# Kernel tuning notes

Measured on AMD Instinct MI355X. Metric: run time of the kernel, lower is better.

## Reference

```python
import jax, jax.numpy as jnp
import numpy as np

H = 2048  # hidden_size
I = 8192  # intermediate_size
B, S = 4, 2048


def setup_inputs() -> dict:
    key = jax.random.key(0)
    ks = jax.random.split(key, 8)
    scale = 1.0 / np.sqrt(H)
    scale_i = 1.0 / np.sqrt(I)
    x = jax.random.normal(ks[0], (B, S, H), dtype=jnp.float32)
    mask = jax.random.randint(ks[1], (B, S), 0, 2) > 0  # bool per-token routing
    # torch nn.Linear weights are [out_features, in_features]
    w1 = jax.random.normal(ks[2], (I, H), dtype=jnp.float32) * scale
    w2 = jax.random.normal(ks[3], (H, I), dtype=jnp.float32) * scale_i
    w3 = jax.random.normal(ks[4], (I, H), dtype=jnp.float32) * scale
    u1 = jax.random.normal(ks[5], (I, H), dtype=jnp.float32) * scale
    u2 = jax.random.normal(ks[6], (H, I), dtype=jnp.float32) * scale_i
    u3 = jax.random.normal(ks[7], (I, H), dtype=jnp.float32) * scale
    return {"x": x, "mask": mask, "w1": w1, "w2": w2, "w3": w3,
            "u1": u1, "u2": u2, "u3": u3}


def reference(x, mask, w1, w2, w3, u1, u2, u3):
    # branch 1 SwiGLU: silu(x @ w1^T) * (x @ w3^T), then w2
    proj1 = jax.nn.silu(jnp.einsum('bsh,ih->bsi', x, w1)) * jnp.einsum('bsh,ih->bsi', x, w3)
    proj2 = jax.nn.silu(jnp.einsum('bsh,ih->bsi', x, u1)) * jnp.einsum('bsh,ih->bsi', x, u3)
    out1 = jnp.einsum('bsi,hi->bsh', proj1, w2)
    out2 = jnp.einsum('bsi,hi->bsh', proj2, u2)
    m = mask[:, :, None]
    return jnp.where(m, out1, out2)
```

## Files before the change

### kernel.cpp

```cpp
#include <hip/hip_runtime.h>
#include <hip/hip_bf16.h>
#include <stdint.h>

#define DIM_H 2048
#define DIM_I 8192
#define TOKENS 8192
#define RB256 34
#define CROWS (RB256*256)

typedef __attribute__((ext_vector_type(8))) short bf16x8;
typedef __attribute__((ext_vector_type(4))) float f32x4;

#define MF(a,b,c) __builtin_amdgcn_mfma_f32_16x16x32_bf16((a),(b),(c),0,0,0)

__device__ __forceinline__ unsigned short f2bf(float f) {
    union { float f; unsigned u; } v; v.f = f;
    return (unsigned short)((v.u + 0x7FFF + ((v.u >> 16) & 1)) >> 16);
}

__global__ __launch_bounds__(256) void cvt_kernel(const float* __restrict__ in,
                                                  unsigned short* __restrict__ out,
                                                  int n4) {
    int stride = gridDim.x * blockDim.x;
    for (int j = blockIdx.x * blockDim.x + threadIdx.x; j < n4; j += stride) {
        float4 v = reinterpret_cast<const float4*>(in)[j];
        ushort4 o;
        o.x = f2bf(v.x); o.y = f2bf(v.y); o.z = f2bf(v.z); o.w = f2bf(v.w);
        reinterpret_cast<ushort4*>(out)[j] = o;
    }
}

__global__ __launch_bounds__(256) void cvt13_kernel(const float* __restrict__ w1,
                                                    const float* __restrict__ w3,
                                                    unsigned short* __restrict__ W13,
                                                    int n4) {
    int stride = gridDim.x * blockDim.x;
    for (int j = blockIdx.x * blockDim.x + threadIdx.x; j < n4; j += stride) {
        int flat = j << 2;
        int R = flat >> 11;
        int col = flat & 2047;
        int orow = ((R >> 4) << 5) | (R & 15);
        float4 v1 = reinterpret_cast<const float4*>(w1)[j];
        float4 v3 = reinterpret_cast<const float4*>(w3)[j];
        ushort4 o1, o3;
        o1.x=f2bf(v1.x); o1.y=f2bf(v1.y); o1.z=f2bf(v1.z); o1.w=f2bf(v1.w);
        o3.x=f2bf(v3.x); o3.y=f2bf(v3.y); o3.z=f2bf(v3.z); o3.w=f2bf(v3.w);
        *reinterpret_cast<ushort4*>(&W13[(size_t)orow * DIM_H + col]) = o1;
        *reinterpret_cast<ushort4*>(&W13[(size_t)(orow + 16) * DIM_H + col]) = o3;
    }
}

__global__ __launch_bounds__(256) void compact_kernel(const int* __restrict__ mask,
                                                      int* __restrict__ idx,
                                                      int* __restrict__ hdr) {
    __shared__ int cnt[256];
    const int t = threadIdx.x;
    const int base = t * 32;
    unsigned bits = 0;
#pragma unroll
    for (int j = 0; j < 32; ++j)
        if (mask[base + j] != 0) bits |= (1u << j);
    const int c = __popc(bits);
    cnt[t] = c;
    __syncthreads();
    for (int off = 1; off < 256; off <<= 1) {
        int v = cnt[t];
        int add = (t >= off) ? cnt[t - off] : 0;
        __syncthreads();
        cnt[t] = v + add;
        __syncthreads();
    }
    const int Mw  = cnt[255];
    const int MwP = (Mw + 255) & ~255;
    const int Mu  = TOKENS - Mw;
    const int MuP = (Mu + 255) & ~255;

    for (int j = t; j < CROWS; j += 256) idx[j] = -1;
    __syncthreads();

    int pw = cnt[t] - c;
    int pz = base - pw;
#pragma unroll
    for (int j = 0; j < 32; ++j) {
        int tok = base + j;
        if ((bits >> j) & 1) idx[pw++] = tok;
        else                 idx[MwP + pz++] = tok;
    }
    if (t == 0) {
        hdr[0] = MwP >> 8;
        hdr[1] = (MwP + MuP) >> 8;
        hdr[2] = Mw;
        hdr[3] = Mu;
    }
}


#define LDF4(D0,D1,D2,D3, SB, RB) do { \
    const unsigned short* _sl = &smem[(SB)]; \
    D0 = *reinterpret_cast<const bf16x8*>(&_sl[((RB) +  0)*32 + c16r]); \
    D1 = *reinterpret_cast<const bf16x8*>(&_sl[((RB) + 16)*32 + c16r]); \
    D2 = *reinterpret_cast<const bf16x8*>(&_sl[((RB) + 32)*32 + c16r]); \
    D3 = *reinterpret_cast<const bf16x8*>(&_sl[((RB) + 48)*32 + c16r]); \
} while(0)

#define STAGE2(UB_, S0_, S1_, KOFS_) do { \
    __builtin_amdgcn_global_load_lds((const __attribute__((address_space(1))) void*)((S0_) + (KOFS_)), \
        (__attribute__((address_space(3))) void*)&smem[(UB_) + wave*512], 16, 0, 0); \
    __builtin_amdgcn_global_load_lds((const __attribute__((address_space(1))) void*)((S1_) + (KOFS_)), \
        (__attribute__((address_space(3))) void*)&smem[(UB_) + 4096 + wave*512], 16, 0, 0); \
} while(0)

#define MFMA32() do { \
  __builtin_amdgcn_s_setprio(1); \
  acc[0][0]=MF(af0,bfr0,acc[0][0]); acc[0][1]=MF(af0,bfr1,acc[0][1]); acc[0][2]=MF(af0,bfr2,acc[0][2]); acc[0][3]=MF(af0,bfr3,acc[0][3]); \
  acc[1][0]=MF(af1,bfr0,acc[1][0]); acc[1][1]=MF(af1,bfr1,acc[1][1]); acc[1][2]=MF(af1,bfr2,acc[1][2]); acc[1][3]=MF(af1,bfr3,acc[1][3]); \
  acc[2][0]=MF(af2,bfr0,acc[2][0]); acc[2][1]=MF(af2,bfr1,acc[2][1]); acc[2][2]=MF(af2,bfr2,acc[2][2]); acc[2][3]=MF(af2,bfr3,acc[2][3]); \
  acc[3][0]=MF(af3,bfr0,acc[3][0]); acc[3][1]=MF(af3,bfr1,acc[3][1]); acc[3][2]=MF(af3,bfr2,acc[3][2]); acc[3][3]=MF(af3,bfr3,acc[3][3]); \
  acc[4][0]=MF(af4,bfr0,acc[4][0]); acc[4][1]=MF(af4,bfr1,acc[4][1]); acc[4][2]=MF(af4,bfr2,acc[4][2]); acc[4][3]=MF(af4,bfr3,acc[4][3]); \
  acc[5][0]=MF(af5,bfr0,acc[5][0]); acc[5][1]=MF(af5,bfr1,acc[5][1]); acc[5][2]=MF(af5,bfr2,acc[5][2]); acc[5][3]=MF(af5,bfr3,acc[5][3]); \
  acc[6][0]=MF(af6,bfr0,acc[6][0]); acc[6][1]=MF(af6,bfr1,acc[6][1]); acc[6][2]=MF(af6,bfr2,acc[6][2]); acc[6][3]=MF(af6,bfr3,acc[6][3]); \
  acc[7][0]=MF(af7,bfr0,acc[7][0]); acc[7][1]=MF(af7,bfr1,acc[7][1]); acc[7][2]=MF(af7,bfr2,acc[7][2]); acc[7][3]=MF(af7,bfr3,acc[7][3]); \
  __builtin_amdgcn_s_setprio(0); \
} while(0)

#define VMB() do { \
    asm volatile("s_waitcnt vmcnt(8)" ::: "memory"); \
    __builtin_amdgcn_s_barrier(); \
} while(0)

#define PHASE(ABASE, BBASE, SA_UB, SB_UB, KO) do { \
    LDF4(af0,af1,af2,af3, (ABASE), rAb); \
    LDF4(af4,af5,af6,af7, (ABASE), rAb + 64); \
    LDF4(bfr0,bfr1,bfr2,bfr3, (BBASE), rBb); \
    STAGE2((SA_UB), sa0, sa1, (KO)); \
    STAGE2((SB_UB), sb0, sb1, (KO)); \
    MFMA32(); \
    VMB(); \
} while(0)

#define KLOOP(NT) do { \
    STAGE2(0,     sa0, sa1, 0);   STAGE2(16384, sb0, sb1, 0);    \
    STAGE2(8192,  sa0, sa1, 32);  STAGE2(24576, sb0, sb1, 32);   \
    STAGE2(32768, sa0, sa1, 64);  STAGE2(49152, sb0, sb1, 64);   \
    VMB(); \
    for (int s = 0; s < (NT)/2; ++s) { \
         \
        PHASE(0,             16384,         32768 + 8192,  32768 + 24576, 96);    \
        PHASE(8192,          24576,         0,             16384,         128);   \
         \
        PHASE(32768,         32768 + 16384, 8192,          24576,         160);   \
        PHASE(32768 + 8192,  32768 + 24576, 32768,         32768 + 16384, 192);   \
        sa0 += 128; sa1 += 128; sb0 += 128; sb1 += 128; \
    } \
} while(0)

__global__ __launch_bounds__(512, 2) void gemm1_kernel(
    const unsigned short* __restrict__ xb,
    const unsigned short* __restrict__ W13,
    const unsigned short* __restrict__ U13,
    const int* __restrict__ idx, const int* __restrict__ hdr,
    unsigned short* __restrict__ P)
{
    __shared__ __align__(16) unsigned short smem[65536];
    const int wB  = hdr[0];
    const int rbT = hdr[1];
    const int nwg = gridDim.x;
    const int q8  = nwg >> 3;
    const int swzb = ((int)blockIdx.x & 7) * q8 + ((int)blockIdx.x >> 3);
    const int rb = swzb % RB256;
    const int bx = swzb / RB256;
    if (rb >= rbT) return;
    const unsigned short* Bm = (rb < wB) ? W13 : U13;
    const int bm0 = rb << 8;
    const int bn0 = bx << 8;

    const int tid  = threadIdx.x;
    const int lane = tid & 63;
    const int wave = tid >> 6;
    const int wrM = wave >> 2;
    const int wcN = wave & 3;
    const int rAb = wrM * 128 + (lane & 15);
    const int rBb = wcN * 64 + (lane & 15);
    const int c16r = (((lane >> 4) ^ ((lane >> 1) & 3))) << 3;

    const int p0 = tid, p1 = 512 + tid;
    const int r0 = p0 >> 2, r1 = p1 >> 2;
    const int c0 = ((p0 & 3) ^ ((r0 >> 1) & 3)) << 3;
    const int c1 = ((p1 & 3) ^ ((r1 >> 1) & 3)) << 3;
    int t0 = idx[bm0 + r0]; if (t0 < 0) t0 = 0;
    int t1 = idx[bm0 + r1]; if (t1 < 0) t1 = 0;
    const unsigned short* sa0 = xb + (size_t)t0 * DIM_H + c0;
    const unsigned short* sa1 = xb + (size_t)t1 * DIM_H + c1;
    const unsigned short* sb0 = Bm + (size_t)(bn0 + r0) * DIM_H + c0;
    const unsigned short* sb1 = Bm + (size_t)(bn0 + r1) * DIM_H + c1;

    f32x4 acc[8][4] = {};
    bf16x8 af0, af1, af2, af3, af4, af5, af6, af7, bfr0, bfr1, bfr2, bfr3;

    KLOOP(32);

    const int crow = (lane >> 4) << 2;
    const int ccol = lane & 15;
    unsigned short* Pw = P + (size_t)(bm0 + wrM * 128) * DIM_I
                           + (size_t)bx * 128 + wcN * 32 + ccol;
#pragma unroll
    for (int m = 0; m < 8; ++m) {
#pragma unroll
        for (int q = 0; q < 2; ++q) {
            f32x4 h1 = acc[m][2 * q];
            f32x4 h3 = acc[m][2 * q + 1];
#pragma unroll
            for (int r = 0; r < 4; ++r) {
                float a = h1[r];
                float p = a * (1.0f / (1.0f + __expf(-a))) * h3[r];
                Pw[(size_t)(m * 16 + crow + r) * DIM_I + q * 16] = f2bf(p);
            }
        }
    }
}

__global__ __launch_bounds__(512, 2) void gemm2_kernel(
    const unsigned short* __restrict__ P,
    const unsigned short* __restrict__ w2b, const unsigned short* __restrict__ u2b,
    const int* __restrict__ idx, const int* __restrict__ hdr,
    float* __restrict__ out)
{
    __shared__ __align__(16) unsigned short smem[65536];
    const int wB  = hdr[0];
    const int rbT = hdr[1];
    const int nwg = gridDim.x;
    const int q8  = nwg >> 3;
    const int swzb = ((int)blockIdx.x & 7) * q8 + ((int)blockIdx.x >> 3);
    const int rb = swzb % RB256;
    const int bx = swzb / RB256;
    if (rb >= rbT) return;
    const unsigned short* Bm = (rb < wB) ? w2b : u2b;
    const int bm0 = rb << 8;
    const int bn0 = bx << 8;

    const int tid  = threadIdx.x;
    const int lane = tid & 63;
    const int wave = tid >> 6;
    const int wrM = wave >> 2;
    const int wcN = wave & 3;
    const int rAb = wrM * 128 + (lane & 15);
    const int rBb = wcN * 64 + (lane & 15);
    const int c16r = (((lane >> 4) ^ ((lane >> 1) & 3))) << 3;

    const int p0 = tid, p1 = 512 + tid;
    const int r0 = p0 >> 2, r1 = p1 >> 2;
    const int c0 = ((p0 & 3) ^ ((r0 >> 1) & 3)) << 3;
    const int c1 = ((p1 & 3) ^ ((r1 >> 1) & 3)) << 3;
    const unsigned short* sa0 = P  + (size_t)(bm0 + r0) * DIM_I + c0;
    const unsigned short* sa1 = P  + (size_t)(bm0 + r1) * DIM_I + c1;
    const unsigned short* sb0 = Bm + (size_t)(bn0 + r0) * DIM_I + c0;
    const unsigned short* sb1 = Bm + (size_t)(bn0 + r1) * DIM_I + c1;

    f32x4 acc[8][4] = {};
    bf16x8 af0, af1, af2, af3, af4, af5, af6, af7, bfr0, bfr1, bfr2, bfr3;

    KLOOP(128);

    const int crow = (lane >> 4) << 2;
    const int ccol = lane & 15;
#pragma unroll
    for (int m = 0; m < 8; ++m) {
#pragma unroll
        for (int r = 0; r < 4; ++r) {
            int rowc = bm0 + wrM * 128 + m * 16 + crow + r;
            int g = idx[rowc];
            if (g >= 0) {
                float* op = out + (size_t)g * DIM_H + bn0 + wcN * 64 + ccol;
#pragma unroll
                for (int n = 0; n < 4; ++n) op[n * 16] = acc[m][n][r];
            }
        }
    }
}

extern "C" void kernel_launch(void* const* d_in, const int* in_sizes, int n_in,
                              void* d_out, int out_size, void* d_ws, size_t ws_size,
                              hipStream_t stream) {
    const float* x    = (const float*)d_in[0];
    const int*   mask = (const int*)d_in[1];
    const float* w1 = (const float*)d_in[2];
    const float* w2 = (const float*)d_in[3];
    const float* w3 = (const float*)d_in[4];
    const float* u1 = (const float*)d_in[5];
    const float* u2 = (const float*)d_in[6];
    const float* u3 = (const float*)d_in[7];
    float* out = (float*)d_out;

    const size_t XN   = (size_t)TOKENS * DIM_H;
    const size_t WN   = (size_t)DIM_I * DIM_H;
    const size_t PN   = (size_t)CROWS * DIM_I;
    const size_t W13N = 2 * WN;

    unsigned short* ws  = (unsigned short*)d_ws;
    unsigned short* xb  = ws;
    unsigned short* Pb  = xb + XN;
    unsigned short* W13 = Pb + PN;
    unsigned short* U13 = W13 + W13N;
    int* idx = (int*)(U13 + W13N);
    int* hdr = idx + CROWS;
    unsigned short* w2b = W13;
    unsigned short* u2b = U13;

    const int cvtBlocks = 2048;
    const int n4 = (int)(WN / 4);

    cvt_kernel  <<<cvtBlocks, 256, 0, stream>>>(x, xb, (int)(XN / 4));
    cvt13_kernel<<<cvtBlocks, 256, 0, stream>>>(w1, w3, W13, n4);
    cvt13_kernel<<<cvtBlocks, 256, 0, stream>>>(u1, u3, U13, n4);
    compact_kernel<<<1, 256, 0, stream>>>(mask, idx, hdr);

    gemm1_kernel<<<64 * RB256, 512, 0, stream>>>(xb, W13, U13, idx, hdr, Pb);

    cvt_kernel<<<cvtBlocks, 256, 0, stream>>>(w2, w2b, n4);
    cvt_kernel<<<cvtBlocks, 256, 0, stream>>>(u2, u2b, n4);

    gemm2_kernel<<<8 * RB256, 512, 0, stream>>>(Pb, w2b, u2b, idx, hdr, out);
}
```

Baseline: 1.099 ms.

## Shrink GEMM M-tile to 128 rows with triple-buffered single-step K pipeline

Both grouped GEMMs now use 128x256 tiles instead of 256x256. Each wave handles 64 rows and holds a 4x4 accumulator block, and the K loop becomes a 3-stage ring that advances one 32-wide step per barrier. LDS use drops to about 72KB, and launch bounds now ask for 4 blocks per CU. The intent is to finer-grain the compacted row padding and raise occupancy and latency hiding, at the cost of lower arithmetic intensity per tile, more B-operand reloads and twice as many barriers per unit of K.

```diff
diff --git a/kernel.cpp b/kernel.cpp
--- a/kernel.cpp
+++ b/kernel.cpp
@@ -6,6 +6,7 @@
 #define DIM_I 8192
 #define TOKENS 8192
 #define RB256 34
+#define RB128 68
 #define CROWS (RB256*256)
 
 typedef __attribute__((ext_vector_type(8))) short bf16x8;
@@ -110,68 +111,57 @@
         (__attribute__((address_space(3))) void*)&smem[(UB_) + 4096 + wave*512], 16, 0, 0); \
 } while(0)
 
-#define MFMA32() do { \
+#define STAGE1(UB_, S0_, KOFS_) \
+    __builtin_amdgcn_global_load_lds((const __attribute__((address_space(1))) void*)((S0_) + (KOFS_)), \
+        (__attribute__((address_space(3))) void*)&smem[(UB_) + wave*512], 16, 0, 0)
+
+#define MFMA16S() do { \
   __builtin_amdgcn_s_setprio(1); \
-  acc[0][0]=MF(af0,bfr0,acc[0][0]); acc[0][1]=MF(af0,bfr1,acc[0][1]); acc[0][2]=MF(af0,bfr2,acc[0][2]); acc[0][3]=MF(af0,bfr3,acc[0][3]); \
-  acc[1][0]=MF(af1,bfr0,acc[1][0]); acc[1][1]=MF(af1,bfr1,acc[1][1]); acc[1][2]=MF(af1,bfr2,acc[1][2]); acc[1][3]=MF(af1,bfr3,acc[1][3]); \
-  acc[2][0]=MF(af2,bfr0,acc[2][0]); acc[2][1]=MF(af2,bfr1,acc[2][1]); acc[2][2]=MF(af2,bfr2,acc[2][2]); acc[2][3]=MF(af2,bfr3,acc[2][3]); \
-  acc[3][0]=MF(af3,bfr0,acc[3][0]); acc[3][1]=MF(af3,bfr1,acc[3][1]); acc[3][2]=MF(af3,bfr2,acc[3][2]); acc[3][3]=MF(af3,bfr3,acc[3][3]); \
-  acc[4][0]=MF(af4,bfr0,acc[4][0]); acc[4][1]=MF(af4,bfr1,acc[4][1]); acc[4][2]=MF(af4,bfr2,acc[4][2]); acc[4][3]=MF(af4,bfr3,acc[4][3]); \
-  acc[5][0]=MF(af5,bfr0,acc[5][0]); acc[5][1]=MF(af5,bfr1,acc[5][1]); acc[5][2]=MF(af5,bfr2,acc[5][2]); acc[5][3]=MF(af5,bfr3,acc[5][3]); \
-  acc[6][0]=MF(af6,bfr0,acc[6][0]); acc[6][1]=MF(af6,bfr1,acc[6][1]); acc[6][2]=MF(af6,bfr2,acc[6][2]); acc[6][3]=MF(af6,bfr3,acc[6][3]); \
-  acc[7][0]=MF(af7,bfr0,acc[7][0]); acc[7][1]=MF(af7,bfr1,acc[7][1]); acc[7][2]=MF(af7,bfr2,acc[7][2]); acc[7][3]=MF(af7,bfr3,acc[7][3]); \
+  acc[0][0]=MF(af0,bf0,acc[0][0]); acc[0][1]=MF(af0,bf1,acc[0][1]); acc[0][2]=MF(af0,bf2,acc[0][2]); acc[0][3]=MF(af0,bf3,acc[0][3]); \
+  acc[1][0]=MF(af1,bf0,acc[1][0]); acc[1][1]=MF(af1,bf1,acc[1][1]); acc[1][2]=MF(af1,bf2,acc[1][2]); acc[1][3]=MF(af1,bf3,acc[1][3]); \
+  acc[2][0]=MF(af2,bf0,acc[2][0]); acc[2][1]=MF(af2,bf1,acc[2][1]); acc[2][2]=MF(af2,bf2,acc[2][2]); acc[2][3]=MF(af2,bf3,acc[2][3]); \
+  acc[3][0]=MF(af3,bf0,acc[3][0]); acc[3][1]=MF(af3,bf1,acc[3][1]); acc[3][2]=MF(af3,bf2,acc[3][2]); acc[3][3]=MF(af3,bf3,acc[3][3]); \
   __builtin_amdgcn_s_setprio(0); \
 } while(0)
 
-#define VMB() do { \
-    asm volatile("s_waitcnt vmcnt(8)" ::: "memory"); \
-    __builtin_amdgcn_s_barrier(); \
-} while(0)
-
-#define PHASE(ABASE, BBASE, SA_UB, SB_UB, KO) do { \
-    LDF4(af0,af1,af2,af3, (ABASE), rAb); \
-    LDF4(af4,af5,af6,af7, (ABASE), rAb + 64); \
-    LDF4(bfr0,bfr1,bfr2,bfr3, (BBASE), rBb); \
-    STAGE2((SA_UB), sa0, sa1, (KO)); \
-    STAGE2((SB_UB), sb0, sb1, (KO)); \
-    MFMA32(); \
-    VMB(); \
-} while(0)
-
-#define KLOOP(NT) do { \
-    STAGE2(0,     sa0, sa1, 0);   STAGE2(16384, sb0, sb1, 0);    \
-    STAGE2(8192,  sa0, sa1, 32);  STAGE2(24576, sb0, sb1, 32);   \
-    STAGE2(32768, sa0, sa1, 64);  STAGE2(49152, sb0, sb1, 64);   \
-    VMB(); \
-    for (int s = 0; s < (NT)/2; ++s) { \
-         \
-        PHASE(0,             16384,         32768 + 8192,  32768 + 24576, 96);    \
-        PHASE(8192,          24576,         0,             16384,         128);   \
-         \
-        PHASE(32768,         32768 + 16384, 8192,          24576,         160);   \
-        PHASE(32768 + 8192,  32768 + 24576, 32768,         32768 + 16384, 192);   \
-        sa0 += 128; sa1 += 128; sb0 += 128; sb1 += 128; \
+#define KLOOP3(NT) do { \
+    STAGE1(0,     sa0, 0);  STAGE2(4096,          sb0, sb1, 0);    \
+    STAGE1(12288, sa0, 32); STAGE2(12288 + 4096,  sb0, sb1, 32);   \
+    asm volatile("s_waitcnt vmcnt(3)" ::: "memory");               \
+    __builtin_amdgcn_s_barrier();                                  \
+    int ko = 64, cb = 0; \
+    for (int t = 0; t < (NT); ++t) { \
+        const int base = cb * 12288; \
+        int nb = base + 24576; if (nb >= 36864) nb -= 36864;       \
+        LDF4(af0,af1,af2,af3, base,        rAb); \
+        LDF4(bf0,bf1,bf2,bf3, base + 4096, rBb); \
+        STAGE1(nb, sa0, ko); STAGE2(nb + 4096, sb0, sb1, ko);      \
+        ko += 32; \
+        MFMA16S(); \
+        asm volatile("s_waitcnt vmcnt(3)" ::: "memory");           \
+        __builtin_amdgcn_s_barrier();                              \
+        cb = (cb == 2) ? 0 : cb + 1; \
     } \
 } while(0)
 
-__global__ __launch_bounds__(512, 2) void gemm1_kernel(
+__global__ __launch_bounds__(512, 4) void gemm1_kernel(
     const unsigned short* __restrict__ xb,
     const unsigned short* __restrict__ W13,
     const unsigned short* __restrict__ U13,
     const int* __restrict__ idx, const int* __restrict__ hdr,
     unsigned short* __restrict__ P)
 {
-    __shared__ __align__(16) unsigned short smem[65536];
-    const int wB  = hdr[0];
-    const int rbT = hdr[1];
+    __shared__ __align__(16) unsigned short smem[36864];
+    const int wB2  = hdr[0] * 2;
+    const int rbT2 = hdr[1] * 2;
     const int nwg = gridDim.x;
     const int q8  = nwg >> 3;
     const int swzb = ((int)blockIdx.x & 7) * q8 + ((int)blockIdx.x >> 3);
-    const int rb = swzb % RB256;
-    const int bx = swzb / RB256;
-    if (rb >= rbT) return;
-    const unsigned short* Bm = (rb < wB) ? W13 : U13;
-    const int bm0 = rb << 8;
+    const int rb = swzb % RB128;
+    const int bx = swzb / RB128;
+    if (rb >= rbT2) return;
+    const unsigned short* Bm = (rb < wB2) ? W13 : U13;
+    const int bm0 = rb << 7;
     const int bn0 = bx << 8;
 
     const int tid  = threadIdx.x;
@@ -179,32 +169,29 @@
     const int wave = tid >> 6;
     const int wrM = wave >> 2;
     const int wcN = wave & 3;
-    const int rAb = wrM * 128 + (lane & 15);
+    const int rAb = wrM * 64 + (lane & 15);
     const int rBb = wcN * 64 + (lane & 15);
     const int c16r = (((lane >> 4) ^ ((lane >> 1) & 3))) << 3;
 
-    const int p0 = tid, p1 = 512 + tid;
-    const int r0 = p0 >> 2, r1 = p1 >> 2;
-    const int c0 = ((p0 & 3) ^ ((r0 >> 1) & 3)) << 3;
-    const int c1 = ((p1 & 3) ^ ((r1 >> 1) & 3)) << 3;
+    const int r0 = tid >> 2, r1 = 128 + r0;
+    const int c0 = ((tid & 3) ^ ((r0 >> 1) & 3)) << 3;
+    const int c1 = ((tid & 3) ^ ((r1 >> 1) & 3)) << 3;
     int t0 = idx[bm0 + r0]; if (t0 < 0) t0 = 0;
-    int t1 = idx[bm0 + r1]; if (t1 < 0) t1 = 0;
     const unsigned short* sa0 = xb + (size_t)t0 * DIM_H + c0;
-    const unsigned short* sa1 = xb + (size_t)t1 * DIM_H + c1;
     const unsigned short* sb0 = Bm + (size_t)(bn0 + r0) * DIM_H + c0;
     const unsigned short* sb1 = Bm + (size_t)(bn0 + r1) * DIM_H + c1;
 
-    f32x4 acc[8][4] = {};
-    bf16x8 af0, af1, af2, af3, af4, af5, af6, af7, bfr0, bfr1, bfr2, bfr3;
-
-    KLOOP(32);
+    f32x4 acc[4][4] = {};
+    bf16x8 af0, af1, af2, af3, bf0, bf1, bf2, bf3;
+
+    KLOOP3(64);
 
     const int crow = (lane >> 4) << 2;
     const int ccol = lane & 15;
-    unsigned short* Pw = P + (size_t)(bm0 + wrM * 128) * DIM_I
+    unsigned short* Pw = P + (size_t)(bm0 + wrM * 64) * DIM_I
                            + (size_t)bx * 128 + wcN * 32 + ccol;
 #pragma unroll
-    for (int m = 0; m < 8; ++m) {
+    for (int m = 0; m < 4; ++m) {
 #pragma unroll
         for (int q = 0; q < 2; ++q) {
             f32x4 h1 = acc[m][2 * q];
@@ -219,23 +206,23 @@
     }
 }
 
-__global__ __launch_bounds__(512, 2) void gemm2_kernel(
+__global__ __launch_bounds__(512, 4) void gemm2_kernel(
     const unsigned short* __restrict__ P,
     const unsigned short* __restrict__ w2b, const unsigned short* __restrict__ u2b,
     const int* __restrict__ idx, const int* __restrict__ hdr,
     float* __restrict__ out)
 {
-    __shared__ __align__(16) unsigned short smem[65536];
-    const int wB  = hdr[0];
-    const int rbT = hdr[1];
+    __shared__ __align__(16) unsigned short smem[36864];
+    const int wB2  = hdr[0] * 2;
+    const int rbT2 = hdr[1] * 2;
     const int nwg = gridDim.x;
     const int q8  = nwg >> 3;
     const int swzb = ((int)blockIdx.x & 7) * q8 + ((int)blockIdx.x >> 3);
-    const int rb = swzb % RB256;
-    const int bx = swzb / RB256;
-    if (rb >= rbT) return;
-    const unsigned short* Bm = (rb < wB) ? w2b : u2b;
-    const int bm0 = rb << 8;
+    const int rb = swzb % RB128;
+    const int bx = swzb / RB128;
+    if (rb >= rbT2) return;
+    const unsigned short* Bm = (rb < wB2) ? w2b : u2b;
+    const int bm0 = rb << 7;
     const int bn0 = bx << 8;
 
     const int tid  = threadIdx.x;
@@ -243,31 +230,29 @@
     const int wave = tid >> 6;
     const int wrM = wave >> 2;
     const int wcN = wave & 3;
-    const int rAb = wrM * 128 + (lane & 15);
+    const int rAb = wrM * 64 + (lane & 15);
     const int rBb = wcN * 64 + (lane & 15);
     const int c16r = (((lane >> 4) ^ ((lane >> 1) & 3))) << 3;
 
-    const int p0 = tid, p1 = 512 + tid;
-    const int r0 = p0 >> 2, r1 = p1 >> 2;
-    const int c0 = ((p0 & 3) ^ ((r0 >> 1) & 3)) << 3;
-    const int c1 = ((p1 & 3) ^ ((r1 >> 1) & 3)) << 3;
+    const int r0 = tid >> 2, r1 = 128 + r0;
+    const int c0 = ((tid & 3) ^ ((r0 >> 1) & 3)) << 3;
+    const int c1 = ((tid & 3) ^ ((r1 >> 1) & 3)) << 3;
     const unsigned short* sa0 = P  + (size_t)(bm0 + r0) * DIM_I + c0;
-    const unsigned short* sa1 = P  + (size_t)(bm0 + r1) * DIM_I + c1;
     const unsigned short* sb0 = Bm + (size_t)(bn0 + r0) * DIM_I + c0;
     const unsigned short* sb1 = Bm + (size_t)(bn0 + r1) * DIM_I + c1;
 
-    f32x4 acc[8][4] = {};
-    bf16x8 af0, af1, af2, af3, af4, af5, af6, af7, bfr0, bfr1, bfr2, bfr3;
-
-    KLOOP(128);
+    f32x4 acc[4][4] = {};
+    bf16x8 af0, af1, af2, af3, bf0, bf1, bf2, bf3;
+
+    KLOOP3(256);
 
     const int crow = (lane >> 4) << 2;
     const int ccol = lane & 15;
 #pragma unroll
-    for (int m = 0; m < 8; ++m) {
+    for (int m = 0; m < 4; ++m) {
 #pragma unroll
         for (int r = 0; r < 4; ++r) {
-            int rowc = bm0 + wrM * 128 + m * 16 + crow + r;
+            int rowc = bm0 + wrM * 64 + m * 16 + crow + r;
             int g = idx[rowc];
             if (g >= 0) {
                 float* op = out + (size_t)g * DIM_H + bn0 + wcN * 64 + ccol;
@@ -314,10 +299,10 @@
     cvt13_kernel<<<cvtBlocks, 256, 0, stream>>>(u1, u3, U13, n4);
     compact_kernel<<<1, 256, 0, stream>>>(mask, idx, hdr);
 
-    gemm1_kernel<<<64 * RB256, 512, 0, stream>>>(xb, W13, U13, idx, hdr, Pb);
+    gemm1_kernel<<<64 * RB128, 512, 0, stream>>>(xb, W13, U13, idx, hdr, Pb);
 
     cvt_kernel<<<cvtBlocks, 256, 0, stream>>>(w2, w2b, n4);
     cvt_kernel<<<cvtBlocks, 256, 0, stream>>>(u2, u2b, n4);
 
-    gemm2_kernel<<<8 * RB256, 512, 0, stream>>>(Pb, w2b, u2b, idx, hdr, out);
-}
+    gemm2_kernel<<<8 * RB128, 512, 0, stream>>>(Pb, w2b, u2b, idx, hdr, out);
+}
```

Measured after the change: 1.087 ms. About the same (-1.1%).
